# Optimization experiments

Hardware: AMD Instinct MI355X
Metric: run time of the kernel (lower is better)

## Reference

```python
import jax, jax.numpy as jnp
import numpy as np

B, S, D, H = 4, 2048, 1024, 16
HS = D // H          # head size 64
DF = 4 * D           # ffn hidden 4096
EPS = 1e-5


def _layer_norm(x, g, b):
    mu = jnp.mean(x, axis=-1, keepdims=True)
    var = jnp.var(x, axis=-1, keepdims=True)
    return (x - mu) * jax.lax.rsqrt(var + EPS) * g + b


def setup_inputs() -> dict:
    key = jax.random.key(0)
    ks = jax.random.split(key, 12)
    s_d = 1.0 / np.sqrt(D)
    s_f = 1.0 / np.sqrt(DF)
    return {
        "x": jax.random.normal(ks[0], (B, S, D), jnp.float32),
        # per-head q/k/v projections, batched over heads: [H, D, HS]
        "wq": jax.random.uniform(ks[1], (H, D, HS), jnp.float32, -s_d, s_d),
        "wk": jax.random.uniform(ks[2], (H, D, HS), jnp.float32, -s_d, s_d),
        "wv": jax.random.uniform(ks[3], (H, D, HS), jnp.float32, -s_d, s_d),
        "proj_w": jax.random.uniform(ks[4], (D, D), jnp.float32, -s_d, s_d),
        "proj_b": jax.random.uniform(ks[5], (D,), jnp.float32, -s_d, s_d),
        "ff1_w": jax.random.uniform(ks[6], (D, DF), jnp.float32, -s_d, s_d),
        "ff1_b": jax.random.uniform(ks[7], (DF,), jnp.float32, -s_d, s_d),
        "ff2_w": jax.random.uniform(ks[8], (DF, D), jnp.float32, -s_f, s_f),
        "ff2_b": jax.random.uniform(ks[9], (D,), jnp.float32, -s_f, s_f),
        "ln1_g": jnp.ones((D,), jnp.float32),
        "ln1_b": jnp.zeros((D,), jnp.float32),
        "ln2_g": jnp.ones((D,), jnp.float32),
        "ln2_b": jnp.zeros((D,), jnp.float32),
    }


def reference(x, wq, wk, wv, proj_w, proj_b, ff1_w, ff1_b, ff2_w, ff2_b,
              ln1_g, ln1_b, ln2_g, ln2_b):
    # --- multi-head causal self-attention on ln1(x), all heads batched ---
    h = _layer_norm(x, ln1_g, ln1_b)                      # [B,S,D]
    q = jnp.einsum("bsd,hde->bhse", h, wq)                # [B,H,S,HS]
    k = jnp.einsum("bsd,hde->bhse", h, wk)
    v = jnp.einsum("bsd,hde->bhse", h, wv)
    scale = HS ** -0.5
    scores = jnp.einsum("bhse,bhte->bhst", q, k) * scale  # [B,H,S,S]
    causal = jnp.tril(jnp.ones((S, S), bool))
    scores = jnp.where(causal, scores, jnp.finfo(scores.dtype).min)
    att = jax.nn.softmax(scores, axis=-1)
    o = jnp.einsum("bhst,bhte->bhse", att, v)             # [B,H,S,HS]
    o = o.transpose(0, 2, 1, 3).reshape(B, S, D)          # concat heads
    sa = o @ proj_w + proj_b
    x = x + sa
    # --- FFN on ln2(x) ---
    h2 = _layer_norm(x, ln2_g, ln2_b)
    ff = jax.nn.relu(h2 @ ff1_w + ff1_b) @ ff2_w + ff2_b
    return x + ff
```

## Files before the change

kernel.cpp:

```cpp
#include <hip/hip_runtime.h>
#include <hip/hip_bf16.h>

#define BB 4
#define SS 2048
#define DD 1024
#define HH 16
#define HSZ 64
#define DFF 4096

typedef short short8 __attribute__((ext_vector_type(8)));
typedef float f32x4 __attribute__((ext_vector_type(4)));
typedef unsigned short us4 __attribute__((ext_vector_type(4)));

#define AS1 __attribute__((address_space(1)))
#define AS3 __attribute__((address_space(3)))

__device__ __forceinline__ unsigned short f2bf(float f) {
    return __bfloat16_as_ushort(__float2bfloat16(f));
}

__global__ __launch_bounds__(256) void pack_qkv_kernel(
    const float* __restrict__ wq, const float* __restrict__ wk,
    const float* __restrict__ wv, __hip_bfloat16* __restrict__ out)
{
    __shared__ float tile[64][65];
    const int bid = blockIdx.x;
    const int kt = bid & 15, hh = (bid >> 4) & 15, sel = bid >> 8;
    const float* src = (sel == 0) ? wq : (sel == 1) ? wk : wv;
    src += (size_t)hh * (DD * HSZ) + (size_t)kt * 64 * HSZ;
    const int tx = threadIdx.x & 63, ty = threadIdx.x >> 6;
    #pragma unroll
    for (int r = 0; r < 64; r += 4)
        tile[r + ty][tx] = src[(size_t)(r + ty) * HSZ + tx];
    __syncthreads();
    unsigned short* o = (unsigned short*)out + (size_t)(sel * DD + hh * 64) * DD + kt * 64;
    #pragma unroll
    for (int r = 0; r < 64; r += 4) {
        int e = r + ty;
        o[(size_t)e * DD + tx] = f2bf(tile[tx][e]);
    }
}

__global__ __launch_bounds__(256) void pack_T_kernel(
    const float* __restrict__ in, __hip_bfloat16* __restrict__ out, int K, int N)
{
    __shared__ float tile[64][65];
    const int nb = N >> 6;
    const int tn0 = (blockIdx.x % nb) << 6, tk0 = (blockIdx.x / nb) << 6;
    const int tx = threadIdx.x & 63, ty = threadIdx.x >> 6;
    #pragma unroll
    for (int r = 0; r < 64; r += 4)
        tile[r + ty][tx] = in[(size_t)(tk0 + r + ty) * N + tn0 + tx];
    __syncthreads();
    unsigned short* o = (unsigned short*)out;
    #pragma unroll
    for (int r = 0; r < 64; r += 4) {
        int n = r + ty;
        o[(size_t)(tn0 + n) * K + tk0 + tx] = f2bf(tile[tx][n]);
    }
}

__global__ __launch_bounds__(256) void ln_kernel(
    const float* __restrict__ x, const float* __restrict__ g,
    const float* __restrict__ b, __hip_bfloat16* __restrict__ out)
{
    int row = blockIdx.x;
    int t = threadIdx.x;
    const float4* xr = (const float4*)(x + (size_t)row * DD);
    float4 v = xr[t];
    float s = v.x + v.y + v.z + v.w;
    float ss = v.x * v.x + v.y * v.y + v.z * v.z + v.w * v.w;
    #pragma unroll
    for (int off = 32; off; off >>= 1) {
        s += __shfl_xor(s, off, 64);
        ss += __shfl_xor(ss, off, 64);
    }
    __shared__ float red[8];
    int w = t >> 6, lane = t & 63;
    if (lane == 0) { red[w] = s; red[4 + w] = ss; }
    __syncthreads();
    s = red[0] + red[1] + red[2] + red[3];
    ss = red[4] + red[5] + red[6] + red[7];
    float mu = s * (1.f / DD);
    float var = ss * (1.f / DD) - mu * mu;
    float rs = rsqrtf(var + 1e-5f);
    float4 gv = ((const float4*)g)[t];
    float4 bv = ((const float4*)b)[t];
    ushort4 pk = make_ushort4(
        f2bf((v.x - mu) * rs * gv.x + bv.x),
        f2bf((v.y - mu) * rs * gv.y + bv.y),
        f2bf((v.z - mu) * rs * gv.z + bv.z),
        f2bf((v.w - mu) * rs * gv.w + bv.w));
    *(ushort4*)((unsigned short*)out + (size_t)row * DD + t * 4) = pk;
}

template<int BN, bool BIAS, bool RELU, bool RES, bool OUTF32>
__global__ __launch_bounds__(512) void gemm_kernel(
    const __hip_bfloat16* __restrict__ A, const __hip_bfloat16* __restrict__ BT,
    const float* __restrict__ bias, const float* __restrict__ res,
    void* __restrict__ Cout, int M, int N, int K, int nbx)
{
    constexpr int NB = BN / 128;
    constexpr int NREP = BN / 64;
    __shared__ uint4 Ah[2][2][1024];
    __shared__ uint4 Bh[2][NB][1024];

    const int tid = threadIdx.x;
    const int lane = tid & 63;
    const int w = tid >> 6;
    const int lr = lane & 15, g = lane >> 4;
    const int nwg = gridDim.x;
    const int cpx = nwg >> 3;
    const int wg = blockIdx.x;
    const int swz = (wg & 7) * cpx + (wg >> 3);
    const int bx = swz % nbx, by = swz / nbx;
    const int row0 = by * 256, col0 = bx * BN;
    const int wm = w >> 2, wn = w & 3;
    const int NT = K >> 6;

    f32x4 acc0[4][NREP] = {};
    f32x4 acc1[4][NREP] = {};
    short8 bfr[NREP][2];

    auto stageA = [&](int buf, int half, int t) {
        const int k0 = t * 64;
        #pragma unroll
        for (int j = 0; j < 2; ++j) {
            int s = j * 512 + tid;
            int r = s >> 3;
            int c = (s & 7) ^ (r & 7);
            const __hip_bfloat16* src = A + (size_t)(row0 + half * 128 + r) * K + k0 + c * 8;
            __builtin_amdgcn_global_load_lds((const AS1 void*)src,
                (AS3 void*)(&Ah[buf][half][j * 512 + (tid & ~63)]), 16, 0, 0);
        }
    };
    auto stageB = [&](int buf, int half, int t) {
        const int k0 = t * 64;
        #pragma unroll
        for (int j = 0; j < 2; ++j) {
            int s = j * 512 + tid;
            int r = s >> 3;
            int c = (s & 7) ^ (r & 7);
            const __hip_bfloat16* src = BT + (size_t)(col0 + half * 128 + r) * K + k0 + c * 8;
            __builtin_amdgcn_global_load_lds((const AS1 void*)src,
                (AS3 void*)(&Bh[buf][half][j * 512 + (tid & ~63)]), 16, 0, 0);
        }
    };
    auto loadB = [&](int buf) {
        const int hb = (NB == 2) ? (wn >> 1) : 0;
        const int cb = (NB == 2) ? ((wn & 1) * 64) : (wn * 32);
        #pragma unroll
        for (int n = 0; n < NREP; ++n) {
            int c = cb + n * 16 + lr;
            #pragma unroll
            for (int kk = 0; kk < 2; ++kk)
                bfr[n][kk] = *(const short8*)&Bh[buf][hb][c * 8 + ((kk * 4 + g) ^ (c & 7))];
        }
    };
    auto phase = [&](auto& acc, int buf, int mh) {
        short8 af[4][2];
        #pragma unroll
        for (int mi = 0; mi < 4; ++mi) {
            int r = wm * 64 + mi * 16 + lr;
            #pragma unroll
            for (int kk = 0; kk < 2; ++kk)
                af[mi][kk] = *(const short8*)&Ah[buf][mh][r * 8 + ((kk * 4 + g) ^ (r & 7))];
        }
        asm volatile("s_waitcnt lgkmcnt(0)" ::: "memory");
        __builtin_amdgcn_sched_barrier(0);
        __builtin_amdgcn_s_setprio(1);
        #pragma unroll
        for (int mi = 0; mi < 4; ++mi)
            #pragma unroll
            for (int n = 0; n < NREP; ++n)
                #pragma unroll
                for (int kk = 0; kk < 2; ++kk)
                    acc[mi][n] = __builtin_amdgcn_mfma_f32_16x16x32_bf16(
                        af[mi][kk], bfr[n][kk], acc[mi][n], 0, 0, 0);
        __builtin_amdgcn_s_setprio(0);
    };

    stageA(0, 0, 0);
    stageB(0, 0, 0);
    if constexpr (NB == 2) stageB(0, 1, 0);
    stageA(0, 1, 0);
    stageA(1, 0, 1);
    if constexpr (NB == 2) stageB(1, 0, 1);

    for (int t = 0; t < NT; ++t) {
        const int buf = t & 1;
        if (t < NT - 1) {
            if constexpr (NB == 2) asm volatile("s_waitcnt vmcnt(4)" ::: "memory");
            else                   asm volatile("s_waitcnt vmcnt(2)" ::: "memory");
        } else {
            asm volatile("s_waitcnt vmcnt(0)" ::: "memory");
        }
        __builtin_amdgcn_s_barrier();
        __builtin_amdgcn_sched_barrier(0);
        if (t + 1 < NT) {
            if constexpr (NB == 2) { stageB(buf ^ 1, 1, t + 1); stageA(buf ^ 1, 1, t + 1); }
            else                   { stageB(buf ^ 1, 0, t + 1); stageA(buf ^ 1, 1, t + 1); }
        }
        loadB(buf);
        phase(acc0, buf, 0);
        if (t < NT - 1) {
            if constexpr (NB == 2) asm volatile("s_waitcnt vmcnt(8)" ::: "memory");
            else                   asm volatile("s_waitcnt vmcnt(6)" ::: "memory");
        } else {
            asm volatile("s_waitcnt vmcnt(0)" ::: "memory");
        }
        __builtin_amdgcn_s_barrier();
        __builtin_amdgcn_sched_barrier(0);
        if (t + 2 < NT) {
            stageA(buf, 0, t + 2);
            if constexpr (NB == 2) stageB(buf, 0, t + 2);
        }
        phase(acc1, buf, 1);
    }

    auto store = [&](auto& acc, int mh) {
        #pragma unroll
        for (int mi = 0; mi < 4; ++mi) {
            #pragma unroll
            for (int j = 0; j < 4; ++j) {
                int rr = row0 + mh * 128 + wm * 64 + mi * 16 + g * 4 + j;
                #pragma unroll
                for (int n = 0; n < NREP; ++n) {
                    int cc = col0 + wn * (NREP * 16) + n * 16 + lr;
                    float vv = acc[mi][n][j];
                    if (BIAS) vv += bias[cc];
                    if (RELU) vv = fmaxf(vv, 0.f);
                    if (RES) vv += res[(size_t)rr * N + cc];
                    if (OUTF32) ((float*)Cout)[(size_t)rr * N + cc] = vv;
                    else ((__hip_bfloat16*)Cout)[(size_t)rr * N + cc] = __float2bfloat16(vv);
                }
            }
        }
    };
    store(acc0, 0);
    store(acc1, 1);
}

__device__ __forceinline__ void stage_K(
    const unsigned short* __restrict__ qkvu, size_t rowbase, int h, int kv0, int tl,
    unsigned short* __restrict__ Kb)
{
    int kv = tl >> 2, c = tl & 3;
    const unsigned short* src = qkvu + rowbase + (size_t)(kv0 + kv) * 3072 + DD + h * HSZ + c * 16;
    uint4 v0 = *(const uint4*)src;
    uint4 v1 = *(const uint4*)(src + 8);
    int sw = kv & 7;
    *(uint4*)&Kb[kv * 64 + ((2 * c) ^ sw) * 8] = v0;
    *(uint4*)&Kb[kv * 64 + ((2 * c + 1) ^ sw) * 8] = v1;
}

__device__ __forceinline__ void stage_V(
    const unsigned short* __restrict__ qkvu, size_t rowbase, int h, int kv0, int tl,
    unsigned short* __restrict__ Vb)
{
    int bkv = ((tl >> 6) << 2) | (tl & 3);
    int bd = (tl >> 2) & 15;
    const unsigned short* src = qkvu + rowbase + (size_t)(kv0 + bkv * 4) * 3072 + 2 * DD + h * HSZ + bd * 4;
    us4 r0 = *(const us4*)src;
    us4 r1 = *(const us4*)(src + 3072);
    us4 r2 = *(const us4*)(src + 2 * 3072);
    us4 r3 = *(const us4*)(src + 3 * 3072);
    #pragma unroll
    for (int cc = 0; cc < 4; ++cc) {
        int d = bd * 4 + cc;
        us4 wv = { r0[cc], r1[cc], r2[cc], r3[cc] };
        *(us4*)&Vb[d * 64 + (((bkv >> 1) ^ (d & 7)) * 8) + (bkv & 1) * 4] = wv;
    }
}

__device__ __forceinline__ void flash_tile(
    const unsigned short* __restrict__ Kb, const unsigned short* __restrict__ Vb,
    unsigned short* __restrict__ Pw, const short8* qfc, int qgc, int kv0, int q, int g,
    float& m_run, float& l_run, f32x4* oacc, bool masked)
{
    f32x4 st[4] = {};
    __builtin_amdgcn_s_setprio(1);
    #pragma unroll
    for (int tt = 0; tt < 4; ++tt) {
        #pragma unroll
        for (int kk = 0; kk < 2; ++kk) {
            short8 kf = *(const short8*)&Kb[(tt * 16 + q) * 64 + ((4 * kk + g) ^ (q & 7)) * 8];
            st[tt] = __builtin_amdgcn_mfma_f32_16x16x32_bf16(kf, qfc[kk], st[tt], 0, 0, 0);
        }
    }
    __builtin_amdgcn_s_setprio(0);

    const float SC = 0.1803368801111731f;
    float mt = -1e30f;
    if (masked) {
        #pragma unroll
        for (int tt = 0; tt < 4; ++tt)
            #pragma unroll
            for (int j = 0; j < 4; ++j) {
                float s = st[tt][j] * SC;
                int kvg = kv0 + tt * 16 + g * 4 + j;
                s = (kvg <= qgc) ? s : -1e30f;
                st[tt][j] = s;
                mt = fmaxf(mt, s);
            }
    } else {
        #pragma unroll
        for (int tt = 0; tt < 4; ++tt)
            #pragma unroll
            for (int j = 0; j < 4; ++j) {
                float s = st[tt][j] * SC;
                st[tt][j] = s;
                mt = fmaxf(mt, s);
            }
    }
    mt = fmaxf(mt, __shfl_xor(mt, 16, 64));
    mt = fmaxf(mt, __shfl_xor(mt, 32, 64));

    bool defer = __all(mt <= m_run + 11.0f);
    if (!defer) {
        float m_new = fmaxf(m_run, mt);
        float corr = exp2f(m_run - m_new);
        #pragma unroll
        for (int j = 0; j < 4; ++j) {
            float cj = __shfl(corr, g * 4 + j, 64);
            #pragma unroll
            for (int dn = 0; dn < 4; ++dn)
                oacc[dn][j] *= cj;
        }
        l_run *= corr;
        m_run = m_new;
    }

    float lsum = 0.f;
    #pragma unroll
    for (int tt = 0; tt < 4; ++tt)
        #pragma unroll
        for (int j = 0; j < 4; ++j) {
            float p = exp2f(st[tt][j] - m_run);
            st[tt][j] = p;
            lsum += p;
        }
    lsum += __shfl_xor(lsum, 16, 64);
    lsum += __shfl_xor(lsum, 32, 64);
    l_run += lsum;

    __builtin_amdgcn_s_setprio(1);
    #pragma unroll
    for (int kk = 0; kk < 2; ++kk) {
        #pragma unroll
        for (int rt = 0; rt < 2; ++rt) {
            int tt = kk * 2 + rt;
            unsigned int lo = ((unsigned int)f2bf(st[tt][1]) << 16) | (unsigned int)f2bf(st[tt][0]);
            unsigned int hi = ((unsigned int)f2bf(st[tt][3]) << 16) | (unsigned int)f2bf(st[tt][2]);
            uint2 pk = make_uint2(lo, hi);
            *(uint2*)&Pw[q * 32 + ((2 * rt + (g >> 1)) ^ ((q >> 1) & 3)) * 8 + (g & 1) * 4] = pk;
        }
        short8 pf = *(const short8*)&Pw[q * 32 + (g ^ ((q >> 1) & 3)) * 8];
        #pragma unroll
        for (int dn = 0; dn < 4; ++dn) {
            short8 vf = *(const short8*)&Vb[(dn * 16 + q) * 64 + ((4 * kk + g) ^ (q & 7)) * 8];
            oacc[dn] = __builtin_amdgcn_mfma_f32_16x16x32_bf16(pf, vf, oacc[dn], 0, 0, 0);
        }
    }
    __builtin_amdgcn_s_setprio(0);
}

__global__ __launch_bounds__(512, 4) void attn_kernel(
    const __hip_bfloat16* __restrict__ qkv, __hip_bfloat16* __restrict__ o)
{
    __shared__ unsigned short K_lds[2][64 * 64];
    __shared__ unsigned short Vt_lds[2][64 * 64];
    __shared__ unsigned short P_lds[8 * 512];

    const int t = threadIdx.x;
    const int lane = t & 63, w = t >> 6;
    const int grp = w >> 2, wq4 = w & 3, tl = t & 255;
    const int q = lane & 15, g = lane >> 4;
    const int wg = blockIdx.x;
    const int swzb = (wg & 7) * 128 + (wg >> 3);
    const int pq = swzb & 15;
    const int h = (swzb >> 4) & 15;
    const int b = swzb >> 8;
    const int qtA = pq, qtB = 31 - pq;
    const int qt1 = grp ? qtB : qtA;
    const unsigned short* qkvu = (const unsigned short*)qkv;
    const size_t rowbase = (size_t)(b * SS) * 3072;
    unsigned short* Kb = K_lds[grp];
    unsigned short* Vb = Vt_lds[grp];
    unsigned short* Pw = &P_lds[w * 512];
    unsigned short* op = (unsigned short*)o;

    int qt_cur = qt1;
    int qgc = qt_cur * 64 + wq4 * 16 + q;
    short8 qfc[2];
    #pragma unroll
    for (int kk = 0; kk < 2; ++kk)
        qfc[kk] = *(const short8*)(qkvu + rowbase + (size_t)qgc * 3072 + h * HSZ + kk * 32 + g * 8);

    f32x4 oacc[4] = {};
    float m_run = -1e30f, l_run = 0.f;

    for (int it = 0; it <= pq; ++it) {
        __syncthreads();
        if (grp == 0) stage_K(qkvu, rowbase, h, it * 64, tl, K_lds[0]);
        else          stage_V(qkvu, rowbase, h, it * 64, tl, Vt_lds[0]);
        __syncthreads();
        flash_tile(K_lds[0], Vt_lds[0], Pw, qfc, qgc, it * 64, q, g, m_run, l_run, oacc,
                   it == qt_cur);
    }

    if (grp == 0) {
        #pragma unroll
        for (int j = 0; j < 4; ++j) {
            float lj = __shfl(l_run, g * 4 + j, 64);
            float inv = 1.f / lj;
            int orow = qtA * 64 + wq4 * 16 + g * 4 + j;
            #pragma unroll
            for (int dn = 0; dn < 4; ++dn)
                op[(size_t)(b * SS + orow) * DD + h * HSZ + dn * 16 + q] = f2bf(oacc[dn][j] * inv);
        }
        qt_cur = qtB;
        qgc = qtB * 64 + wq4 * 16 + q;
        #pragma unroll
        for (int kk = 0; kk < 2; ++kk)
            qfc[kk] = *(const short8*)(qkvu + rowbase + (size_t)qgc * 3072 + h * HSZ + kk * 32 + g * 8);
        m_run = -1e30f; l_run = 0.f;
        #pragma unroll
        for (int dn = 0; dn < 4; ++dn) oacc[dn] = f32x4{0.f, 0.f, 0.f, 0.f};
    }

    for (int it2 = 0; it2 < 16 - pq; ++it2) {
        int tile = grp ? (pq + 1 + it2) : (16 + it2);
        bool active = grp ? (tile <= 15) : true;
        __syncthreads();
        if (active) {
            stage_K(qkvu, rowbase, h, tile * 64, tl, Kb);
            stage_V(qkvu, rowbase, h, tile * 64, tl, Vb);
        }
        __syncthreads();
        if (active) flash_tile(Kb, Vb, Pw, qfc, qgc, tile * 64, q, g, m_run, l_run, oacc,
                               tile == qt_cur);
    }

    __syncthreads();
    float* obuf = (float*)K_lds;
    float* mlbuf = (float*)P_lds;
    if (grp == 0) {
        #pragma unroll
        for (int dn = 0; dn < 4; ++dn)
            #pragma unroll
            for (int j = 0; j < 4; ++j)
                obuf[wq4 * 1024 + lane * 16 + dn * 4 + j] = oacc[dn][j];
        if (g == 0) { mlbuf[wq4 * 32 + q] = m_run; mlbuf[wq4 * 32 + 16 + q] = l_run; }
    }
    __syncthreads();
    if (grp == 1) {
        float mA = mlbuf[wq4 * 32 + q];
        float lA = mlbuf[wq4 * 32 + 16 + q];
        float mM = fmaxf(m_run, mA);
        float sB = exp2f(m_run - mM);
        float sA = exp2f(mA - mM);
        float lM = l_run * sB + lA * sA;
        #pragma unroll
        for (int j = 0; j < 4; ++j) {
            float sBj = __shfl(sB, g * 4 + j, 64);
            float sAj = __shfl(sA, g * 4 + j, 64);
            float lMj = __shfl(lM, g * 4 + j, 64);
            float inv = 1.f / lMj;
            int orow = qtB * 64 + wq4 * 16 + g * 4 + j;
            #pragma unroll
            for (int dn = 0; dn < 4; ++dn) {
                float oA = obuf[wq4 * 1024 + lane * 16 + dn * 4 + j];
                float vv = (oacc[dn][j] * sBj + oA * sAj) * inv;
                op[(size_t)(b * SS + orow) * DD + h * HSZ + dn * 16 + q] = f2bf(vv);
            }
        }
    }
}

extern "C" void kernel_launch(void* const* d_in, const int* in_sizes, int n_in,
                              void* d_out, int out_size, void* d_ws, size_t ws_size,
                              hipStream_t stream)
{
    const float* x      = (const float*)d_in[0];
    const float* wq     = (const float*)d_in[1];
    const float* wk     = (const float*)d_in[2];
    const float* wv     = (const float*)d_in[3];
    const float* proj_w = (const float*)d_in[4];
    const float* proj_b = (const float*)d_in[5];
    const float* ff1_w  = (const float*)d_in[6];
    const float* ff1_b  = (const float*)d_in[7];
    const float* ff2_w  = (const float*)d_in[8];
    const float* ff2_b  = (const float*)d_in[9];
    const float* ln1_g  = (const float*)d_in[10];
    const float* ln1_b  = (const float*)d_in[11];
    const float* ln2_g  = (const float*)d_in[12];
    const float* ln2_b  = (const float*)d_in[13];
    float* out = (float*)d_out;

    char* ws = (char*)d_ws;
    const size_t MB = 1ull << 20;
    __hip_bfloat16* h     = (__hip_bfloat16*)(ws);
    __hip_bfloat16* qkv   = (__hip_bfloat16*)(ws + 16 * MB);
    __hip_bfloat16* obuf  = (__hip_bfloat16*)(ws + 64 * MB);
    float*          x1    = (float*)(ws + 80 * MB);
    __hip_bfloat16* wqkvT = (__hip_bfloat16*)(ws + 112 * MB);
    __hip_bfloat16* projT = (__hip_bfloat16*)(ws + 118 * MB);
    __hip_bfloat16* ff1T  = (__hip_bfloat16*)(ws + 120 * MB);
    __hip_bfloat16* ff2T  = (__hip_bfloat16*)(ws + 128 * MB);
    __hip_bfloat16* f1    = (__hip_bfloat16*)(ws + 16 * MB);

    const int ROWS = BB * SS;

    pack_qkv_kernel<<<768, 256, 0, stream>>>(wq, wk, wv, wqkvT);
    pack_T_kernel<<<(DD / 64) * (DD / 64), 256, 0, stream>>>(proj_w, projT, DD, DD);
    pack_T_kernel<<<(DFF / 64) * (DD / 64), 256, 0, stream>>>(ff1_w, ff1T, DD, DFF);
    pack_T_kernel<<<(DD / 64) * (DFF / 64), 256, 0, stream>>>(ff2_w, ff2T, DFF, DD);

    ln_kernel<<<ROWS, 256, 0, stream>>>(x, ln1_g, ln1_b, h);
    gemm_kernel<128, false, false, false, false><<<(ROWS / 256) * (3 * DD / 128), 512, 0, stream>>>(
        h, wqkvT, nullptr, nullptr, qkv, ROWS, 3 * DD, DD, 3 * DD / 128);
    attn_kernel<<<BB * HH * 16, 512, 0, stream>>>(qkv, obuf);
    gemm_kernel<128, true, false, true, true><<<(ROWS / 256) * (DD / 128), 512, 0, stream>>>(
        obuf, projT, proj_b, x, x1, ROWS, DD, DD, DD / 128);
    ln_kernel<<<ROWS, 256, 0, stream>>>(x1, ln2_g, ln2_b, h);
    gemm_kernel<256, true, true, false, false><<<(ROWS / 256) * (DFF / 256), 512, 0, stream>>>(
        h, ff1T, ff1_b, nullptr, f1, ROWS, DFF, DD, DFF / 256);
    gemm_kernel<128, true, false, true, true><<<(ROWS / 256) * (DD / 128), 512, 0, stream>>>(
        f1, ff2T, ff2_b, x1, out, ROWS, DD, DFF, DD / 128);
}
```

Baseline: 415.7 us.

## Add dedicated 256x256 GEMM kernel with staggered B prefetch for FFN1

Adds a specialized 256x256-tile bf16 MFMA GEMM for the FFN up-projection. It splits each k-tile into four phases of 32 rows, and interleaves prefetch of the next A tile and the B tile two steps ahead between phases, using direct global-to-LDS loads. Each wave holds a 128x64 output fragment, loads its B fragments once per k-tile and reuses them across all four phases. The aim is to overlap memory traffic with MFMA work and to cut LDS reads. The cost is higher register pressure (128 accumulator floats per thread) and more barriers.

Measured after the change: 418.3 us. No clear change (+0.6%).

```diff
diff --git a/kernel.cpp b/kernel.cpp
--- a/kernel.cpp
+++ b/kernel.cpp
@@ -241,6 +241,126 @@
     store(acc1, 1);
 }
 
+template<bool BIAS, bool RELU, bool RES, bool OUTF32>
+__global__ __launch_bounds__(512) void gemm256_kernel(
+    const __hip_bfloat16* __restrict__ A, const __hip_bfloat16* __restrict__ BT,
+    const float* __restrict__ bias, const float* __restrict__ res,
+    void* __restrict__ Cout, int M, int N, int K, int nbx)
+{
+    __shared__ uint4 Ah[2][2][1024];
+    __shared__ uint4 Bh[2][2][1024];
+    const int tid = threadIdx.x, lane = tid & 63, w = tid >> 6;
+    const int lr = lane & 15, g = lane >> 4;
+    const int nwg = gridDim.x, cpx = nwg >> 3, wg = blockIdx.x;
+    const int swz = (wg & 7) * cpx + (wg >> 3);
+    const int bx = swz % nbx, by = swz / nbx;
+    const int row0 = by * 256, col0 = bx * 256;
+    const int wm = w >> 2, wn = w & 3;
+    const int NT = K >> 6;
+    f32x4 acc[8][4] = {};
+    short8 bfr[4][2];
+
+    auto stA = [&](int buf, int half, int t) {
+        const int k0 = t * 64;
+        #pragma unroll
+        for (int j = 0; j < 2; ++j) {
+            int s = j * 512 + tid;
+            int r = s >> 3, c = (s & 7) ^ (r & 7);
+            const __hip_bfloat16* src = A + (size_t)(row0 + half * 128 + r) * K + k0 + c * 8;
+            __builtin_amdgcn_global_load_lds((const AS1 void*)src,
+                (AS3 void*)(&Ah[buf][half][j * 512 + (tid & ~63)]), 16, 0, 0);
+        }
+    };
+    auto stB = [&](int buf, int half, int t) {
+        const int k0 = t * 64;
+        #pragma unroll
+        for (int j = 0; j < 2; ++j) {
+            int s = j * 512 + tid;
+            int r = s >> 3, c = (s & 7) ^ (r & 7);
+            const __hip_bfloat16* src = BT + (size_t)(col0 + half * 128 + r) * K + k0 + c * 8;
+            __builtin_amdgcn_global_load_lds((const AS1 void*)src,
+                (AS3 void*)(&Bh[buf][half][j * 512 + (tid & ~63)]), 16, 0, 0);
+        }
+    };
+    auto loadB = [&](int buf) {
+        #pragma unroll
+        for (int n = 0; n < 4; ++n) {
+            int c = wn * 64 + n * 16 + lr;
+            int hb = c >> 7, rr = c & 127;
+            #pragma unroll
+            for (int kk = 0; kk < 2; ++kk)
+                bfr[n][kk] = *(const short8*)&Bh[buf][hb][rr * 8 + ((kk * 4 + g) ^ (rr & 7))];
+        }
+    };
+    auto phase = [&](int buf, int p) {
+        short8 af[2][2];
+        #pragma unroll
+        for (int m2 = 0; m2 < 2; ++m2) {
+            int r = p * 32 + m2 * 16 + lr;
+            #pragma unroll
+            for (int kk = 0; kk < 2; ++kk)
+                af[m2][kk] = *(const short8*)&Ah[buf][wm][r * 8 + ((kk * 4 + g) ^ (r & 7))];
+        }
+        asm volatile("s_waitcnt lgkmcnt(0)" ::: "memory");
+        __builtin_amdgcn_sched_barrier(0);
+        __builtin_amdgcn_s_setprio(1);
+        #pragma unroll
+        for (int m2 = 0; m2 < 2; ++m2)
+            #pragma unroll
+            for (int n = 0; n < 4; ++n)
+                #pragma unroll
+                for (int kk = 0; kk < 2; ++kk)
+                    acc[p * 2 + m2][n] = __builtin_amdgcn_mfma_f32_16x16x32_bf16(
+                        af[m2][kk], bfr[n][kk], acc[p * 2 + m2][n], 0, 0, 0);
+        __builtin_amdgcn_s_setprio(0);
+    };
+
+    stB(0, 0, 0); stB(0, 1, 0);
+    stA(0, 0, 0); stA(0, 1, 0);
+    stB(1, 0, 1); stB(1, 1, 1);
+
+    for (int t = 0; t < NT; ++t) {
+        const int buf = t & 1;
+        if (t + 1 < NT) asm volatile("s_waitcnt vmcnt(4)" ::: "memory");
+        else            asm volatile("s_waitcnt vmcnt(0)" ::: "memory");
+        __builtin_amdgcn_s_barrier();
+        __builtin_amdgcn_sched_barrier(0);
+        if (t + 1 < NT) { stA(buf ^ 1, 0, t + 1); stA(buf ^ 1, 1, t + 1); }
+        loadB(buf);
+        phase(buf, 0);
+        __builtin_amdgcn_s_barrier();
+        __builtin_amdgcn_sched_barrier(0);
+        if (t + 2 < NT) stB(buf, 0, t + 2);
+        phase(buf, 1);
+        __builtin_amdgcn_s_barrier();
+        __builtin_amdgcn_sched_barrier(0);
+        if (t + 2 < NT) stB(buf, 1, t + 2);
+        phase(buf, 2);
+        __builtin_amdgcn_s_barrier();
+        __builtin_amdgcn_sched_barrier(0);
+        phase(buf, 3);
+        __builtin_amdgcn_s_barrier();
+    }
+
+    #pragma unroll
+    for (int mi = 0; mi < 8; ++mi) {
+        #pragma unroll
+        for (int j = 0; j < 4; ++j) {
+            int rr = row0 + wm * 128 + mi * 16 + g * 4 + j;
+            #pragma unroll
+            for (int n = 0; n < 4; ++n) {
+                int cc = col0 + wn * 64 + n * 16 + lr;
+                float vv = acc[mi][n][j];
+                if (BIAS) vv += bias[cc];
+                if (RELU) vv = fmaxf(vv, 0.f);
+                if (RES) vv += res[(size_t)rr * N + cc];
+                if (OUTF32) ((float*)Cout)[(size_t)rr * N + cc] = vv;
+                else ((__hip_bfloat16*)Cout)[(size_t)rr * N + cc] = __float2bfloat16(vv);
+            }
+        }
+    }
+}
+
 __device__ __forceinline__ void stage_K(
     const unsigned short* __restrict__ qkvu, size_t rowbase, int h, int kv0, int tl,
     unsigned short* __restrict__ Kb)
@@ -524,7 +644,7 @@
     gemm_kernel<128, true, false, true, true><<<(ROWS / 256) * (DD / 128), 512, 0, stream>>>(
         obuf, projT, proj_b, x, x1, ROWS, DD, DD, DD / 128);
     ln_kernel<<<ROWS, 256, 0, stream>>>(x1, ln2_g, ln2_b, h);
-    gemm_kernel<256, true, true, false, false><<<(ROWS / 256) * (DFF / 256), 512, 0, stream>>>(
+    gemm256_kernel<true, true, false, false><<<(ROWS / 256) * (DFF / 256), 512, 0, stream>>>(
         h, ff1T, ff1_b, nullptr, f1, ROWS, DFF, DD, DFF / 256);
     gemm_kernel<128, true, false, true, true><<<(ROWS / 256) * (DD / 128), 512, 0, stream>>>(
         f1, ff2T, ff2_b, x1, out, ROWS, DD, DFF, DD / 128);
```
